# Optimization experiments

Hardware: AMD Instinct MI355X
Metric: run time of the kernel (lower is better)

The kernel has to match this reference:

```python
import jax, jax.numpy as jnp
import numpy as np

N_USERS = 20000
N_ITEMS = 30000
N = N_USERS + N_ITEMS          # total nodes
D = 64                          # embedding_dim
EXTRA = 1152                    # 768 metadata + 384 review
E = 500000                      # full-graph edges
NC = 100                        # clusters
HEADS = 2                       # per-layer GATConv heads
CG_HEADS = 4                    # GlobalGATOverClusters hard-codes heads=4
L = 2                           # num_layers
ED = 2                          # edge_dim


def _gat(x, ei, ea, lin, a_src, a_dst, lin_e, a_edge, bias, heads, nnodes):
    """PyG GATConv: add self loops (edge_attr fill='mean'), concat=False -> head mean."""
    C = a_src.shape[-1]
    loop = jnp.arange(nnodes)
    src = jnp.concatenate([ei[0], loop])
    dst = jnp.concatenate([ei[1], loop])
    ea_full = jnp.concatenate([ea, jnp.broadcast_to(ea.mean(0), (nnodes, ea.shape[1]))], 0)
    xh = (x @ lin).reshape(nnodes, heads, C)            # [N,H,C]
    asrc = (xh * a_src).sum(-1)                         # [N,H]
    adst = (xh * a_dst).sum(-1)
    eh = (ea_full @ lin_e).reshape(-1, heads, C)        # [Etot,H,C]
    ae = (eh * a_edge).sum(-1)                          # [Etot,H]
    al = jax.nn.leaky_relu(asrc[src] + adst[dst] + ae, 0.2)
    amax = jax.ops.segment_max(al, dst, num_segments=nnodes)
    ex = jnp.exp(al - amax[dst])
    s = jax.ops.segment_sum(ex, dst, num_segments=nnodes)
    w = ex / (s[dst] + 1e-16)
    out = jax.ops.segment_sum(xh[src] * w[..., None], dst, num_segments=nnodes)
    return out.mean(1) + bias


def _graph_norm(x, weight, bias, mean_scale, eps=1e-5):
    mean = x.mean(0)
    out = x - mean_scale * mean
    var = (out * out).mean(0)
    return weight * out * jax.lax.rsqrt(var + eps) + bias


def _forward(product_extra_features, user_emb, item_emb, fus_w1, fus_b1, fus_w2, fus_b2,
             full_edge_attr, gcn_w, gcn_b,
             cg_lin, cg_att_src, cg_att_dst, cg_lin_edge, cg_att_edge, cg_bias, cluster_edge_attr,
             gat_lin, gat_att_src, gat_att_dst, gat_lin_edge, gat_att_edge, gat_bias,
             gn_weight, gn_bias, gn_mean_scale,
             full_edge_index, cluster_assignment, cluster_edge_index):
    # fusion MLP on item side (dropout is identity at inference)
    h = jnp.maximum(jnp.concatenate([item_emb, product_extra_features], -1) @ fus_w1 + fus_b1, 0.0)
    enriched_items = h @ fus_w2 + fus_b2
    X = jnp.concatenate([user_emb, enriched_items], 0)  # [N, D]

    # per-cluster GCN == one GCN over intra-cluster edges + self loops;
    # nodes in clusters with zero intra edges keep original features
    ei0, ei1 = full_edge_index[0], full_edge_index[1]
    intra = cluster_assignment[ei0] == cluster_assignment[ei1]
    loop = jnp.arange(N)
    row = jnp.concatenate([ei0, loop])
    col = jnp.concatenate([ei1, loop])
    ew = jnp.concatenate([intra.astype(X.dtype), jnp.ones((N,), X.dtype)])
    deg = jax.ops.segment_sum(ew, col, num_segments=N)
    dinv = jnp.where(deg > 0, jax.lax.rsqrt(deg), 0.0)
    norm = dinv[row] * ew * dinv[col]
    xw = X @ gcn_w
    gcn_out = jax.ops.segment_sum(xw[row] * norm[:, None], col, num_segments=N) + gcn_b
    cl_has_edge = jax.ops.segment_sum(intra.astype(jnp.int32), cluster_assignment[ei0], num_segments=NC) > 0
    Xc = jnp.where(cl_has_edge[cluster_assignment][:, None], gcn_out, X)

    # mean pool per cluster
    cnt = jax.ops.segment_sum(jnp.ones((N,), X.dtype), cluster_assignment, num_segments=NC)
    pooled = jax.ops.segment_sum(Xc, cluster_assignment, num_segments=NC) / jnp.maximum(cnt, 1.0)[:, None]

    # global GAT over clusters (inter-cluster multigraph, precomputed)
    cl_upd = _gat(pooled, cluster_edge_index, cluster_edge_attr,
                  cg_lin, cg_att_src, cg_att_dst, cg_lin_edge, cg_att_edge, cg_bias, CG_HEADS, NC)
    Xcomb = Xc + cl_upd[cluster_assignment]

    # full-graph GAT stack with GraphNorm + residual ELU (dropout identity)
    for i in range(L):
        Xin = Xcomb
        g = _gat(Xcomb, full_edge_index, full_edge_attr,
                 gat_lin[i], gat_att_src[i], gat_att_dst[i],
                 gat_lin_edge[i], gat_att_edge[i], gat_bias[i], HEADS, N)
        g = _graph_norm(g, gn_weight[i], gn_bias[i], gn_mean_scale[i])
        Xcomb = jax.nn.elu(g + Xin)

    return Xcomb[:N_USERS], Xcomb[N_USERS:]


def setup_inputs() -> dict:
    rng = np.random.default_rng(0)
    fei = rng.integers(0, N, size=(2, E)).astype(np.int32)
    ca = rng.integers(0, NC, size=(N,)).astype(np.int32)
    fea = rng.random((E, ED)).astype(np.float32)
    # build_cluster_graph: one cluster edge per inter-cluster full edge
    cu, cv = ca[fei[0]], ca[fei[1]]
    m = cu != cv
    cei = np.stack([cu[m], cv[m]]).astype(np.int32)
    cea = fea[m]

    key = jax.random.key(0)
    ks = jax.random.split(key, 24)
    nrm = lambda k, shp, s=0.05: jax.random.normal(k, shp, dtype=jnp.float32) * s
    return {
        'product_extra_features': jax.random.normal(ks[0], (N_ITEMS, EXTRA), dtype=jnp.float32),
        'user_emb': nrm(ks[1], (N_USERS, D), 1.0),
        'item_emb': nrm(ks[2], (N_ITEMS, D), 1.0),
        'fus_w1': nrm(ks[3], (D + EXTRA, 2 * D)),
        'fus_b1': jnp.zeros((2 * D,), jnp.float32),
        'fus_w2': nrm(ks[4], (2 * D, D)),
        'fus_b2': jnp.zeros((D,), jnp.float32),
        'full_edge_attr': jnp.asarray(fea),
        'gcn_w': nrm(ks[5], (D, D)),
        'gcn_b': jnp.zeros((D,), jnp.float32),
        'cg_lin': nrm(ks[6], (D, CG_HEADS * D)),
        'cg_att_src': nrm(ks[7], (CG_HEADS, D)),
        'cg_att_dst': nrm(ks[8], (CG_HEADS, D)),
        'cg_lin_edge': nrm(ks[9], (ED, CG_HEADS * D)),
        'cg_att_edge': nrm(ks[10], (CG_HEADS, D)),
        'cg_bias': jnp.zeros((D,), jnp.float32),
        'cluster_edge_attr': jnp.asarray(cea),
        'gat_lin': nrm(ks[11], (L, D, HEADS * D)),
        'gat_att_src': nrm(ks[12], (L, HEADS, D)),
        'gat_att_dst': nrm(ks[13], (L, HEADS, D)),
        'gat_lin_edge': nrm(ks[14], (L, ED, HEADS * D)),
        'gat_att_edge': nrm(ks[15], (L, HEADS, D)),
        'gat_bias': jnp.zeros((L, D), jnp.float32),
        'gn_weight': jnp.ones((L, D), jnp.float32),
        'gn_bias': jnp.zeros((L, D), jnp.float32),
        'gn_mean_scale': jnp.ones((L, D), jnp.float32),
        'full_edge_index': jnp.asarray(fei),
        'cluster_assignment': jnp.asarray(ca),
        'cluster_edge_index': jnp.asarray(cei),
    }


def reference(product_extra_features, user_emb, item_emb, fus_w1, fus_b1, fus_w2, fus_b2,
              full_edge_attr, gcn_w, gcn_b,
              cg_lin, cg_att_src, cg_att_dst, cg_lin_edge, cg_att_edge, cg_bias, cluster_edge_attr,
              gat_lin, gat_att_src, gat_att_dst, gat_lin_edge, gat_att_edge, gat_bias,
              gn_weight, gn_bias, gn_mean_scale,
              full_edge_index, cluster_assignment, cluster_edge_index):
    return _forward(product_extra_features, user_emb, item_emb, fus_w1, fus_b1, fus_w2, fus_b2,
                    full_edge_attr, gcn_w, gcn_b,
                    cg_lin, cg_att_src, cg_att_dst, cg_lin_edge, cg_att_edge, cg_bias, cluster_edge_attr,
                    gat_lin, gat_att_src, gat_att_dst, gat_lin_edge, gat_att_edge, gat_bias,
                    gn_weight, gn_bias, gn_mean_scale,
                    full_edge_index, cluster_assignment, cluster_edge_index)
```

## Files before the change

### kernel.cpp

```cpp
#include <hip/hip_runtime.h>
#include <hip/hip_bf16.h>

#define N_USERS 20000
#define N_ITEMS 30000
#define NTOT    50000
#define DIM     64
#define EXTRA_D 1152
#define E_EDGES 500000
#define NC      100
#define KTOT    1216
#define KSTEPS  38
#define PPART   16

#define FEI_BLKS 128
#define CEI_BLKS 64
#define FILL_BLKS ((E_EDGES+255)/256)
#define DEG_BLKS ((NTOT+3)/4)

typedef __attribute__((ext_vector_type(8))) short short8;
typedef __attribute__((ext_vector_type(4))) float v4f;

__device__ __forceinline__ float wred_sum(float v){
#pragma unroll
  for(int o=32;o;o>>=1) v += __shfl_xor(v,o,64);
  return v;
}
__device__ __forceinline__ int wred_sumi(int v){
#pragma unroll
  for(int o=32;o;o>>=1) v += __shfl_xor(v,o,64);
  return v;
}
__device__ __forceinline__ float lrelu(float x){ return x>0.f? x : 0.2f*x; }
__device__ __forceinline__ short f2bf(float f){
  unsigned u=__float_as_uint(f);
  unsigned r=(u + 0x7FFFu + ((u>>16)&1u))>>16;
  return (short)r;
}

__global__ __launch_bounds__(256) void prep_misc_kernel(
    const float* __restrict__ u, float* __restrict__ X,
    const float* __restrict__ w1, short* __restrict__ w1t,
    const float* __restrict__ w2, short* __restrict__ w2t,
    const int* __restrict__ ca, int* __restrict__ ccnt)
{
  __shared__ int hist[NC];
  const int b=blockIdx.x, t=threadIdx.x;
  if(b < 1250){
    int i = b*256+t;
    ((float4*)X)[i] = ((const float4*)u)[i];
  } else if(b < 1858){
    int i = (b-1250)*256+t;
    int s = i>>12, rem = i&4095, n = rem>>5, kk = rem&31;
    w1t[i] = f2bf(w1[(s*32+kk)*128 + n]);
  } else if(b < 1890){
    int i = (b-1858)*256+t;
    int c = i>>7, n = i&127;
    w2t[i] = f2bf(w2[n*64+c]);
  } else {
    for(int i=t;i<NC;i+=256) hist[i]=0;
    __syncthreads();
    for(int n=(b-1890)*256+t; n<NTOT; n+=64*256) atomicAdd(&hist[ca[n]],1);
    __syncthreads();
    for(int i=t;i<NC;i+=256) if(hist[i]) atomicAdd(&ccnt[i],hist[i]);
  }
}

__global__ __launch_bounds__(256) void fusion_mfma_kernel(
    const float* __restrict__ item, const float* __restrict__ extra,
    const short* __restrict__ w1t, const float* __restrict__ b1,
    const short* __restrict__ w2t, const float* __restrict__ b2,
    float* __restrict__ X)
{
  __shared__ short As[128*40];
  __shared__ short Bs[128*40];
  __shared__ short Hs[128*136];
  const int tid = threadIdx.x;
  const int blk = blockIdx.x;
  const int w = tid>>6, lane = tid&63, quad = lane>>4, l16 = lane&15;
  const int mw = w&1, nw = w>>1;

  v4f acc[4][4];
#pragma unroll
  for(int a=0;a<4;a++)
#pragma unroll
    for(int b=0;b<4;b++) acc[a][b] = (v4f){0.f,0.f,0.f,0.f};

  const int arow = tid>>3;
  const int aoff = (tid&7)*4;
  for(int s=0;s<KSTEPS;s++){
    const int k0 = s*32;
#pragma unroll
    for(int it=0;it<4;it++){
      int r = arow + it*32;
      int col = k0 + aoff;
      int gr = blk*128 + r; if(gr >= N_ITEMS) gr = N_ITEMS-1;
      float4 v = (col < DIM) ? *(const float4*)(item + (size_t)gr*DIM + col)
                             : *(const float4*)(extra + (size_t)gr*EXTRA_D + (col-DIM));
      short4 bv; bv.x=f2bf(v.x); bv.y=f2bf(v.y); bv.z=f2bf(v.z); bv.w=f2bf(v.w);
      *(short4*)&As[r*40 + aoff] = bv;
    }
#pragma unroll
    for(int it=0;it<2;it++){
      int idx = tid + it*256;
      int4 v = *(const int4*)(w1t + (size_t)s*4096 + idx*8);
      int n = idx>>2, kk = (idx&3)*8;
      *(int4*)&Bs[n*40 + kk] = v;
    }
    __syncthreads();
    short8 af[4], bf_[4];
#pragma unroll
    for(int i=0;i<4;i++){
      int m = mw*64 + i*16 + l16;
      af[i]  = *(const short8*)&As[m*40 + quad*8];
      int n = nw*64 + i*16 + l16;
      bf_[i] = *(const short8*)&Bs[n*40 + quad*8];
    }
#pragma unroll
    for(int mi=0;mi<4;mi++)
#pragma unroll
      for(int ni=0;ni<4;ni++)
        acc[mi][ni] = __builtin_amdgcn_mfma_f32_16x16x32_bf16(af[mi], bf_[ni], acc[mi][ni], 0,0,0);
    __syncthreads();
  }

#pragma unroll
  for(int ni=0;ni<4;ni++){
    int n = nw*64 + ni*16 + l16;
    float bias = b1[n];
#pragma unroll
    for(int mi=0;mi<4;mi++){
      int mbase = mw*64 + mi*16 + quad*4;
#pragma unroll
      for(int r=0;r<4;r++){
        float hv = fmaxf(acc[mi][ni][r] + bias, 0.f);
        Hs[(mbase+r)*136 + n] = f2bf(hv);
      }
    }
  }
  __syncthreads();

  v4f acc2[2][4];
#pragma unroll
  for(int a=0;a<2;a++)
#pragma unroll
    for(int b=0;b<4;b++) acc2[a][b] = (v4f){0.f,0.f,0.f,0.f};
#pragma unroll
  for(int ks=0;ks<4;ks++){
    short8 ha[2];
#pragma unroll
    for(int mi=0;mi<2;mi++){
      int m = w*32 + mi*16 + l16;
      ha[mi] = *(const short8*)&Hs[m*136 + ks*32 + quad*8];
    }
#pragma unroll
    for(int ni=0;ni<4;ni++){
      int c = ni*16 + l16;
      short8 wb = *(const short8*)(w2t + c*128 + ks*32 + quad*8);
#pragma unroll
      for(int mi=0;mi<2;mi++)
        acc2[mi][ni] = __builtin_amdgcn_mfma_f32_16x16x32_bf16(ha[mi], wb, acc2[mi][ni], 0,0,0);
    }
  }
#pragma unroll
  for(int ni=0;ni<4;ni++){
    int c = ni*16 + l16;
    float b2v = b2[c];
#pragma unroll
    for(int mi=0;mi<2;mi++){
      int mbase = w*32 + mi*16 + quad*4;
#pragma unroll
      for(int r=0;r<4;r++){
        int row = blk*128 + mbase + r;
        if(row < N_ITEMS) X[(size_t)(N_USERS+row)*64 + c] = acc2[mi][ni][r] + b2v;
      }
    }
  }
}

__global__ __launch_bounds__(256) void edge_pass_kernel(
    const int* __restrict__ fei, const float* __restrict__ fea, const int* __restrict__ ca,
    int* __restrict__ cnt_dst, int* __restrict__ clflag, float2* __restrict__ partA,
    const int* __restrict__ cei, const float* __restrict__ cea, int Ec,
    int* __restrict__ ccnt_dst, float2* __restrict__ partB)
{
  __shared__ int hist[NC];
  __shared__ float2 w4[4];
  const int b=blockIdx.x, t=threadIdx.x;
  const int lane=t&63, wv=t>>6;
  if(b < FEI_BLKS){
    float a0=0.f,a1=0.f;
    for(int e=b*256+t; e<E_EDGES; e+=FEI_BLKS*256){
      int s=fei[e], d=fei[E_EDGES+e];
      atomicAdd(&cnt_dst[d],1);
      int cs=ca[s];
      if(cs==ca[d]) clflag[cs]=1;
      float2 v=*(const float2*)(fea+2*e);
      a0+=v.x; a1+=v.y;
    }
    a0=wred_sum(a0); a1=wred_sum(a1);
    if(lane==0) w4[wv]=make_float2(a0,a1);
    __syncthreads();
    if(t==0){ float2 r=w4[0]; for(int i=1;i<4;i++){r.x+=w4[i].x; r.y+=w4[i].y;} partA[b]=r; }
  } else {
    int bb=b-FEI_BLKS;
    for(int i=t;i<NC;i+=256) hist[i]=0;
    __syncthreads();
    float a0=0.f,a1=0.f;
    for(int e=bb*256+t; e<Ec; e+=CEI_BLKS*256){
      atomicAdd(&hist[cei[Ec+e]],1);
      float2 v=*(const float2*)(cea+2*e);
      a0+=v.x; a1+=v.y;
    }
    a0=wred_sum(a0); a1=wred_sum(a1);
    if(lane==0) w4[wv]=make_float2(a0,a1);
    __syncthreads();
    if(t==0){ float2 r=w4[0]; for(int i=1;i<4;i++){r.x+=w4[i].x; r.y+=w4[i].y;} partB[bb]=r; }
    for(int i=t;i<NC;i+=256) if(hist[i]) atomicAdd(&ccnt_dst[i],hist[i]);
  }
}

__global__ void prep_small_kernel(const float2* __restrict__ partA, const float2* __restrict__ partB,
    int Ec,
    const float* __restrict__ cg_le, const float* __restrict__ cg_ae,
    const float* __restrict__ gat_le, const float* __restrict__ gat_ae,
    float* __restrict__ coefs)
{
  int tid=threadIdx.x; int lane=tid&63; int wv=tid>>6;
  {
    int hh=wv;
    float v0 = cg_le[hh*64+lane]*cg_ae[hh*64+lane];
    float v1 = cg_le[256 + hh*64+lane]*cg_ae[hh*64+lane];
    v0=wred_sum(v0); v1=wred_sum(v1);
    if(lane==0){ coefs[8+hh]=v0; coefs[12+hh]=v1; }
  }
  {
    int l=wv>>1, hh=wv&1;
    float v0 = gat_le[l*256 + hh*64+lane]     * gat_ae[l*128+hh*64+lane];
    float v1 = gat_le[l*256 + 128 + hh*64+lane]* gat_ae[l*128+hh*64+lane];
    v0=wred_sum(v0); v1=wred_sum(v1);
    if(lane==0){ coefs[16+l*2+hh]=v0; coefs[20+l*2+hh]=v1; }
  }
  __syncthreads();
  if(wv==0){
    float2 v=partA[lane], v2=partA[64+lane];
    float sx=wred_sum(v.x+v2.x), sy=wred_sum(v.y+v2.y);
    if(lane==0){ coefs[4]=sx/(float)E_EDGES; coefs[5]=sy/(float)E_EDGES; }
  }
  if(wv==1){
    float2 v=partB[lane];
    float sx=wred_sum(v.x), sy=wred_sum(v.y);
    if(lane==0){ coefs[6]=sx/(float)Ec; coefs[7]=sy/(float)Ec; }
  }
}

__global__ __launch_bounds__(1024) void scan1_kernel(const int* __restrict__ cnt,
    int* __restrict__ incl, int* __restrict__ bsum){
  __shared__ int s[1024];
  int i = blockIdx.x*1024 + threadIdx.x;
  int v = (i<NTOT)? cnt[i]+1 : 0;
  s[threadIdx.x]=v; __syncthreads();
  for(int off=1; off<1024; off<<=1){
    int t = (threadIdx.x>=off)? s[threadIdx.x-off] : 0;
    __syncthreads();
    s[threadIdx.x]+=t;
    __syncthreads();
  }
  if(i<NTOT) incl[i]=s[threadIdx.x];
  if(threadIdx.x==1023) bsum[blockIdx.x]=s[1023];
}
__global__ void small_scans_kernel(int* __restrict__ bsum, int nb,
    const int* __restrict__ ccnt_dst, int* __restrict__ coffs, int* __restrict__ cfillp){
  int lane=threadIdx.x;
  if(blockIdx.x==0){
    int v = (lane<nb)? bsum[lane]:0;
#pragma unroll
    for(int o=1;o<64;o<<=1){ int t=__shfl_up(v,o,64); if(lane>=o) v+=t; }
    if(lane<nb) bsum[lane]=v;
  } else {
    int v0 = (2*lane<NC)? ccnt_dst[2*lane]:0;
    int v1 = (2*lane+1<NC)? ccnt_dst[2*lane+1]:0;
    int pair=v0+v1;
    int sc=pair;
#pragma unroll
    for(int o=1;o<64;o<<=1){ int t2=__shfl_up(sc,o,64); if(lane>=o) sc+=t2; }
    int excl = sc - pair;
    if(2*lane<NC){ coffs[2*lane]=excl; cfillp[2*lane]=excl; }
    if(2*lane+1<NC){ coffs[2*lane+1]=excl+v0; cfillp[2*lane+1]=excl+v0; }
    if(lane==63) coffs[NC]=sc;
  }
}
__global__ void scan3_kernel(const int* __restrict__ incl, const int* __restrict__ cnt,
    const int* __restrict__ bsum, int* __restrict__ offs, int* __restrict__ fillptr,
    const float* __restrict__ coefs, int4* __restrict__ slot){
  int i=blockIdx.x*256+threadIdx.x;
  if(i<NTOT){
    int blk=i>>10;
    int prev = blk? bsum[blk-1]:0;
    int c=cnt[i];
    int start = prev + incl[i] - (c+1);
    offs[i]=start; fillptr[i]=start;
    slot[start+c]=make_int4(i,__float_as_int(coefs[4]),__float_as_int(coefs[5]),0);
  }
  if(i==0) offs[NTOT]=E_EDGES+NTOT;
}
__global__ __launch_bounds__(256) void fill_both_kernel(
    const int* __restrict__ fei, const float* __restrict__ fea,
    int* __restrict__ fillptr, int4* __restrict__ slot,
    const int* __restrict__ cei, const float* __restrict__ cea, int Ec,
    int* __restrict__ cfillp, int* __restrict__ cslot_src, float2* __restrict__ cslot_ea)
{
  __shared__ int hist[NC];
  __shared__ int base[NC];
  const int b=blockIdx.x, t=threadIdx.x;
  if(b<FILL_BLKS){
    int e=b*256+t;
    if(e<E_EDGES){
      int dst=fei[E_EDGES+e], src=fei[e];
      int pos=atomicAdd(&fillptr[dst],1);
      float2 v=*(const float2*)(fea+2*e);
      slot[pos]=make_int4(src,__float_as_int(v.x),__float_as_int(v.y),0);
    }
  } else {
    int bb=b-FILL_BLKS;
    const int chunk=(Ec+127)/128;
    const int beg=bb*chunk;
    const int end=min(beg+chunk,Ec);
    for(int i=t;i<NC;i+=256) hist[i]=0;
    __syncthreads();
    for(int e=beg+t;e<end;e+=256) atomicAdd(&hist[cei[Ec+e]],1);
    __syncthreads();
    for(int i=t;i<NC;i+=256){
      int h=hist[i];
      base[i] = h ? atomicAdd(&cfillp[i],h) : 0;
      hist[i]=0;
    }
    __syncthreads();
    for(int e=beg+t;e<end;e+=256){
      int d=cei[Ec+e];
      int pos = base[d] + atomicAdd(&hist[d],1);
      cslot_src[pos]=cei[e];
      cslot_ea[pos]=make_float2(cea[2*e],cea[2*e+1]);
    }
  }
}

__global__ __launch_bounds__(256) void gcn_pre_kernel(const int* __restrict__ offs,
    const int4* __restrict__ slot, const int* __restrict__ ca, float* __restrict__ dinv,
    const float* __restrict__ X, const float* __restrict__ gw, float* __restrict__ xw){
  __shared__ float Wl[64*64];
  __shared__ float rowb[4][64];
  const int b=blockIdx.x;
  const int lane=threadIdx.x&63, wv=threadIdx.x>>6;
  if(b<DEG_BLKS){
    int n = b*4+wv; if(n>=NTOT) return;
    int beg=offs[n], end=offs[n+1], myca=ca[n];
    int c=0;
    for(int j=beg+lane;j<end;j+=64) c += (ca[slot[j].x]==myca)?1:0;
    c = wred_sumi(c);
    if(lane==0) dinv[n]=rsqrtf((float)c);
  } else {
    int bb=b-DEG_BLKS;
    for(int i=threadIdx.x;i<4096;i+=256) Wl[i]=gw[i];
    __syncthreads();
    for(int r=bb*4+wv; r<NTOT; r+=1024*4){
      rowb[wv][lane]=X[(size_t)r*64+lane];
      float acc=0.f;
#pragma unroll 8
      for(int k=0;k<64;k++) acc+=rowb[wv][k]*Wl[k*64+lane];
      xw[(size_t)r*64+lane]=acc;
    }
  }
}
__global__ __launch_bounds__(256) void gcn_agg_kernel(const float* __restrict__ X,
    const float* __restrict__ xw, const float* __restrict__ gcn_b,
    const int* __restrict__ offs, const int4* __restrict__ slot, const int* __restrict__ ca,
    const float* __restrict__ dinv, const int* __restrict__ flag,
    float* __restrict__ Xc, float* __restrict__ psum){
  __shared__ float2 stg[4][64];
  int lane=threadIdx.x&63, wv=threadIdx.x>>6;
  int n=blockIdx.x*4+wv; if(n>=NTOT) return;
  int beg=offs[n], end=offs[n+1], myca=ca[n];
  float acc=0.f;
  for(int c0=beg;c0<end;c0+=64){
    int j=c0+lane;
    float coef=0.f; int s=0;
    if(j<end){
      s=slot[j].x;
      if(ca[s]==myca) coef=dinv[s];
    }
    stg[wv][lane]=make_float2(__int_as_float(s),coef);
    unsigned long long bal=__ballot(coef!=0.f);
    while(bal){
      int k=__builtin_ctzll(bal); bal&=bal-1;
      float2 sc=stg[wv][k];
      acc += sc.y * xw[(size_t)__float_as_int(sc.x)*64+lane];
    }
  }
  float gout = dinv[n]*acc + gcn_b[lane];
  float xc = flag[myca] ? gout : X[(size_t)n*64+lane];
  Xc[(size_t)n*64+lane]=xc;
  atomicAdd(&psum[(size_t)(blockIdx.x&(PPART-1))*NC*64 + myca*64+lane], xc);
}

__global__ __launch_bounds__(256) void cluster_prep_kernel(const float* __restrict__ psum,
    const int* __restrict__ ccnt, const float* __restrict__ cg_lin,
    const float* __restrict__ as_, const float* __restrict__ ad_,
    float* __restrict__ xh_c, float* __restrict__ asrc_c, float* __restrict__ adst_c){
  __shared__ float prow[64];
  const int c=blockIdx.x, t=threadIdx.x;
  if(t<64){
    float a=0.f;
#pragma unroll
    for(int p=0;p<PPART;p++) a += psum[(size_t)p*NC*64 + c*64 + t];
    prow[t]=a/fmaxf((float)ccnt[c],1.f);
  }
  __syncthreads();
  float acc=0.f;
#pragma unroll 8
  for(int k=0;k<64;k++) acc += prow[k]*cg_lin[k*256+t];
  xh_c[c*256+t]=acc;
  int lane=t&63, hh=t>>6;
  float s=wred_sum(acc*as_[hh*64+lane]);
  float d=wred_sum(acc*ad_[hh*64+lane]);
  if(lane==0){ asrc_c[c*4+hh]=s; adst_c[c*4+hh]=d; }
}
__global__ __launch_bounds__(256) void cluster_agg_kernel(
    const int* __restrict__ coffs, const int* __restrict__ cslot_src, const float2* __restrict__ cslot_ea,
    const float* __restrict__ asrc_c, const float* __restrict__ adst_c, const float* __restrict__ coefs,
    const float* __restrict__ xh_c, const float* __restrict__ cg_bias, float* __restrict__ cl_upd)
{
  __shared__ float sas[NC*4];
  __shared__ float sW[NC*4];
  __shared__ float ssum[4];
  __shared__ float red[4][64];
  const int c=blockIdx.x, t=threadIdx.x;
  for(int i=t;i<NC*4;i+=256){ sas[i]=asrc_c[i]; sW[i]=0.f; }
  __syncthreads();
  float ad[4], A0[4], A1[4];
#pragma unroll
  for(int h=0;h<4;h++){ ad[h]=adst_c[c*4+h]; A0[h]=coefs[8+h]; A1[h]=coefs[12+h]; }
  const int beg=coffs[c], end=coffs[c+1];
  for(int j=beg+t;j<end;j+=256){
    int s=cslot_src[j]; float2 e=cslot_ea[j];
#pragma unroll
    for(int h=0;h<4;h++){
      float al=lrelu(sas[s*4+h]+ad[h]+e.x*A0[h]+e.y*A1[h]);
      atomicAdd(&sW[s*4+h], expf(al));
    }
  }
  if(t<4){
    float al=lrelu(sas[c*4+t]+ad[t]+coefs[6]*A0[t]+coefs[7]*A1[t]);
    atomicAdd(&sW[c*4+t], expf(al));
  }
  __syncthreads();
  const int h=t>>6, lane=t&63;
  float p=0.f;
  if(lane<NC)    p += sW[lane*4+h];
  if(lane+64<NC) p += sW[(lane+64)*4+h];
  p=wred_sum(p);
  if(lane==0) ssum[h]=p+1e-16f;
  __syncthreads();
  float inv=1.f/ssum[h];
  float acc=0.f;
  for(int s=0;s<NC;s++) acc += sW[s*4+h]*xh_c[s*256+h*64+lane];
  red[h][lane]=acc*inv;
  __syncthreads();
  if(t<64) cl_upd[c*64+t]=0.25f*(red[0][t]+red[1][t]+red[2][t]+red[3][t])+cg_bias[t];
}

__global__ __launch_bounds__(256) void gat_xh0_kernel(const float* __restrict__ Xc,
    const float* __restrict__ cl_upd, const int* __restrict__ ca,
    const float* __restrict__ lin, const float* __restrict__ att_s, const float* __restrict__ att_d,
    float2* __restrict__ xh2, float* __restrict__ asrc, float* __restrict__ adst,
    float* __restrict__ Xa){
  __shared__ __align__(16) float Wl[64*128];
  __shared__ float rowb[4][64];
  int t=threadIdx.x;
  for(int i=t;i<8192;i+=256) Wl[i]=lin[i];
  __syncthreads();
  int lane=t&63, wv=t>>6;
  float as0=att_s[lane], as1=att_s[64+lane], ad0=att_d[lane], ad1=att_d[64+lane];
  for(int r=blockIdx.x*4+wv; r<NTOT; r+=gridDim.x*4){
    float xv = Xc[(size_t)r*64+lane] + cl_upd[ca[r]*64+lane];
    Xa[(size_t)r*64+lane]=xv;
    rowb[wv][lane]=xv;
    float x0=0.f,x1=0.f;
#pragma unroll 8
    for(int k=0;k<64;k++){ float q=rowb[wv][k]; x0+=q*Wl[k*128+lane]; x1+=q*Wl[k*128+64+lane]; }
    xh2[(size_t)r*64+lane]=make_float2(x0,x1);
    float p0=wred_sum(x0*as0);
    float p1=wred_sum(x1*as1);
    float q0=wred_sum(x0*ad0);
    float q1=wred_sum(x1*ad1);
    if(lane==0){ asrc[2*r]=p0; asrc[2*r+1]=p1; adst[2*r]=q0; adst[2*r+1]=q1; }
  }
}
__global__ __launch_bounds__(256) void gat_xh1_kernel(const float* __restrict__ g,
    const float* __restrict__ Xres, const float* __restrict__ stats,
    const float* __restrict__ gnw, const float* __restrict__ gnb, const float* __restrict__ gnms,
    const float* __restrict__ lin, const float* __restrict__ att_s, const float* __restrict__ att_d,
    float2* __restrict__ xh2, float* __restrict__ asrc, float* __restrict__ adst,
    float* __restrict__ Xb){
  __shared__ __align__(16) float Wl[64*128];
  __shared__ float rowb[4][64];
  int t=threadIdx.x;
  for(int i=t;i<8192;i+=256) Wl[i]=lin[i];
  __syncthreads();
  int lane=t&63, wv=t>>6;
  const float invN = 1.f/(float)NTOT;
  float m=stats[lane]*invN;
  float mm=gnms[lane]*m;
  float gwv=rsqrtf(stats[64+lane]*invN - 2.f*mm*m + mm*mm + 1e-5f)*gnw[lane];
  float gbv=gnb[lane];
  float as0=att_s[lane], as1=att_s[64+lane], ad0=att_d[lane], ad1=att_d[64+lane];
  for(int r=blockIdx.x*4+wv; r<NTOT; r+=gridDim.x*4){
    float z=(g[(size_t)r*64+lane]-mm)*gwv+gbv + Xres[(size_t)r*64+lane];
    float xv = z>0.f? z : expf(z)-1.f;
    Xb[(size_t)r*64+lane]=xv;
    rowb[wv][lane]=xv;
    float x0=0.f,x1=0.f;
#pragma unroll 8
    for(int k=0;k<64;k++){ float q=rowb[wv][k]; x0+=q*Wl[k*128+lane]; x1+=q*Wl[k*128+64+lane]; }
    xh2[(size_t)r*64+lane]=make_float2(x0,x1);
    float p0=wred_sum(x0*as0);
    float p1=wred_sum(x1*as1);
    float q0=wred_sum(x0*ad0);
    float q1=wred_sum(x1*ad1);
    if(lane==0){ asrc[2*r]=p0; asrc[2*r+1]=p1; adst[2*r]=q0; adst[2*r+1]=q1; }
  }
}

__global__ __launch_bounds__(256) void gat_agg_kernel(const float2* __restrict__ xh2,
    const float2* __restrict__ asrc, const float2* __restrict__ adst,
    const int* __restrict__ offs, const int4* __restrict__ slot,
    const float* __restrict__ coefs, int layer, const float* __restrict__ bias,
    float* __restrict__ g){
  __shared__ float4 stg[4][64];
  int lane=threadIdx.x&63, wv=threadIdx.x>>6;
  int n=blockIdx.x*4+wv; if(n>=NTOT) return;
  float A00=coefs[16+layer*2+0], A01=coefs[16+layer*2+1];
  float A10=coefs[20+layer*2+0], A11=coefs[20+layer*2+1];
  int beg=offs[n], end=offs[n+1];
  float2 adn=adst[n];
  float s0=0.f,s1=0.f,acc0=0.f,acc1=0.f;
  for(int c0=beg;c0<end;c0+=64){
    int j=c0+lane;
    float ex0=0.f,ex1=0.f; int s=0;
    if(j<end){
      int4 sl=slot[j];
      s=sl.x;
      float e0=__int_as_float(sl.y), e1=__int_as_float(sl.z);
      float2 a=asrc[s];
      ex0=expf(lrelu(a.x+adn.x+e0*A00+e1*A10));
      ex1=expf(lrelu(a.y+adn.y+e0*A01+e1*A11));
    }
    s0+=ex0; s1+=ex1;
    stg[wv][lane]=make_float4(__int_as_float(s),ex0,ex1,0.f);
    int cnt=min(64,end-c0);
    int k=0;
    for(; k+4<=cnt; k+=4){
      float4 w0=stg[wv][k], w1=stg[wv][k+1], w2=stg[wv][k+2], w3=stg[wv][k+3];
      float2 x0=xh2[(size_t)__float_as_int(w0.x)*64+lane];
      float2 x1=xh2[(size_t)__float_as_int(w1.x)*64+lane];
      float2 x2=xh2[(size_t)__float_as_int(w2.x)*64+lane];
      float2 x3=xh2[(size_t)__float_as_int(w3.x)*64+lane];
      acc0 += w0.y*x0.x + w1.y*x1.x + w2.y*x2.x + w3.y*x3.x;
      acc1 += w0.z*x0.y + w1.z*x1.y + w2.z*x2.y + w3.z*x3.y;
    }
    for(; k<cnt; k++){
      float4 ws=stg[wv][k];
      float2 xv=xh2[(size_t)__float_as_int(ws.x)*64+lane];
      acc0 += ws.y*xv.x;
      acc1 += ws.z*xv.y;
    }
  }
  s0=wred_sum(s0); s1=wred_sum(s1);
  g[(size_t)n*64+lane]=0.5f*(acc0/(s0+1e-16f)+acc1/(s1+1e-16f))+bias[lane];
}
__global__ __launch_bounds__(256) void stats_kernel(const float* __restrict__ g,
    float* __restrict__ stats){
  __shared__ float s1[64], s2[64];
  int t=threadIdx.x;
  if(t<64){s1[t]=0.f;s2[t]=0.f;}
  __syncthreads();
  float a0=0.f,a1=0.f,a2=0.f,a3=0.f,b0=0.f,b1=0.f,b2=0.f,b3=0.f;
  int i0=blockIdx.x*256+t;
  for(int i=i0;i<NTOT*16;i+=gridDim.x*256){
    float4 v=((const float4*)g)[i];
    a0+=v.x;a1+=v.y;a2+=v.z;a3+=v.w;
    b0+=v.x*v.x;b1+=v.y*v.y;b2+=v.z*v.z;b3+=v.w*v.w;
  }
  int d0=(i0&15)*4;
  atomicAdd(&s1[d0],a0); atomicAdd(&s1[d0+1],a1); atomicAdd(&s1[d0+2],a2); atomicAdd(&s1[d0+3],a3);
  atomicAdd(&s2[d0],b0); atomicAdd(&s2[d0+1],b1); atomicAdd(&s2[d0+2],b2); atomicAdd(&s2[d0+3],b3);
  __syncthreads();
  if(t<64) atomicAdd(&stats[t],s1[t]);
  else if(t<128) atomicAdd(&stats[t],s2[t-64]);
}
__global__ __launch_bounds__(256) void gnorm_elu_kernel(const float* __restrict__ g,
    const float* __restrict__ Xin, const float* __restrict__ stats,
    const float* __restrict__ gw, const float* __restrict__ gb, const float* __restrict__ gms,
    float* __restrict__ outp){
  const float invN = 1.f/(float)NTOT;
  int i0=blockIdx.x*256+threadIdx.x;
  int d0=(i0&15)*4;
  float mmv[4],gwv[4],gbv[4];
#pragma unroll
  for(int j=0;j<4;j++){
    int d=d0+j;
    float m=stats[d]*invN;
    float mm=gms[d]*m;
    mmv[j]=mm;
    gwv[j]=rsqrtf(stats[64+d]*invN-2.f*mm*m+mm*mm+1e-5f)*gw[d];
    gbv[j]=gb[d];
  }
  for(int i=i0;i<NTOT*16;i+=gridDim.x*256){
    float4 gv=((const float4*)g)[i];
    float4 xv=((const float4*)Xin)[i];
    float4 o; float z;
    z=(gv.x-mmv[0])*gwv[0]+gbv[0]+xv.x; o.x = z>0.f? z : expf(z)-1.f;
    z=(gv.y-mmv[1])*gwv[1]+gbv[1]+xv.y; o.y = z>0.f? z : expf(z)-1.f;
    z=(gv.z-mmv[2])*gwv[2]+gbv[2]+xv.z; o.z = z>0.f? z : expf(z)-1.f;
    z=(gv.w-mmv[3])*gwv[3]+gbv[3]+xv.w; o.w = z>0.f? z : expf(z)-1.f;
    ((float4*)outp)[i]=o;
  }
}

extern "C" void kernel_launch(void* const* d_in, const int* in_sizes, int n_in,
                              void* d_out, int out_size, void* d_ws, size_t ws_size,
                              hipStream_t stream)
{
  const float* extra = (const float*)d_in[0];
  const float* user  = (const float*)d_in[1];
  const float* item  = (const float*)d_in[2];
  const float* fw1 = (const float*)d_in[3];
  const float* fb1 = (const float*)d_in[4];
  const float* fw2 = (const float*)d_in[5];
  const float* fb2 = (const float*)d_in[6];
  const float* fea = (const float*)d_in[7];
  const float* gcn_w = (const float*)d_in[8];
  const float* gcn_b = (const float*)d_in[9];
  const float* cg_lin = (const float*)d_in[10];
  const float* cg_as = (const float*)d_in[11];
  const float* cg_ad = (const float*)d_in[12];
  const float* cg_le = (const float*)d_in[13];
  const float* cg_ae = (const float*)d_in[14];
  const float* cg_bias = (const float*)d_in[15];
  const float* cea = (const float*)d_in[16];
  const float* gat_lin = (const float*)d_in[17];
  const float* gat_as = (const float*)d_in[18];
  const float* gat_ad = (const float*)d_in[19];
  const float* gat_le = (const float*)d_in[20];
  const float* gat_ae = (const float*)d_in[21];
  const float* gat_bias = (const float*)d_in[22];
  const float* gn_w = (const float*)d_in[23];
  const float* gn_b = (const float*)d_in[24];
  const float* gn_ms = (const float*)d_in[25];
  const int* fei = (const int*)d_in[26];
  const int* ca  = (const int*)d_in[27];
  const int* cei = (const int*)d_in[28];
  const int Ec = in_sizes[16]/2;
  float* outp = (float*)d_out;

  char* w = (char*)d_ws;
  auto alloc=[&](size_t b)->char*{ char* p=w; w += (b+255)&~(size_t)255; return p; };

  char* z0 = w;
  int* cnt_dst = (int*)alloc((size_t)NTOT*4);
  int* clflag = (int*)alloc(NC*4);
  int* ccnt = (int*)alloc(NC*4);
  int* ccnt_dst = (int*)alloc(NC*4);
  float* psum = (float*)alloc((size_t)PPART*NC*64*4);
  float* stats0 = (float*)alloc(128*4);
  float* stats1 = (float*)alloc(128*4);
  size_t zbytes = (size_t)(w - z0);

  float2* partA = (float2*)alloc(128*8);
  float2* partB = (float2*)alloc(64*8);
  float* coefs = (float*)alloc(32*4);
  int* offs = (int*)alloc((size_t)(NTOT+1)*4);
  int* incl = (int*)alloc((size_t)NTOT*4);
  int* bsum = (int*)alloc(64*4);
  int* fillptr = (int*)alloc((size_t)NTOT*4);
  int4* slot = (int4*)alloc((size_t)(E_EDGES+NTOT)*16);
  int* coffs = (int*)alloc((size_t)(NC+1)*4);
  int* cfillp = (int*)alloc((size_t)NC*4);
  int* cslot_src = (int*)alloc((size_t)E_EDGES*4);
  float2* cslot_ea = (float2*)alloc((size_t)E_EDGES*8);
  float* dinv = (float*)alloc((size_t)NTOT*4);
  float* xh_c = (float*)alloc(NC*256*4);
  float* asrc_c = (float*)alloc(NC*4*4);
  float* adst_c = (float*)alloc(NC*4*4);
  float* cl_upd = (float*)alloc(NC*64*4);
  float* asrc = (float*)alloc((size_t)NTOT*2*4);
  float* adst = (float*)alloc((size_t)NTOT*2*4);
  short* w1t = (short*)alloc((size_t)KSTEPS*4096*2);
  short* w2t = (short*)alloc((size_t)64*128*2);
  float* bufA = (float*)alloc((size_t)NTOT*64*4);
  float* bufB = (float*)alloc((size_t)NTOT*64*4);
  float* bufC = (float*)alloc((size_t)NTOT*64*4);
  float* bufD = (float*)alloc((size_t)NTOT*64*4);
  float* bufE = (float*)alloc((size_t)NTOT*128*4);

  float* X  = bufA; float* g  = bufA;
  float* Xc = bufB;
  float* xw = bufC; float* Xb = bufC;
  float* Xa = bufD;
  float2* xh2 = (float2*)bufE;

  hipMemsetAsync(z0, 0, zbytes, stream);

  prep_misc_kernel<<<1954,256,0,stream>>>(user, X, fw1, w1t, fw2, w2t, ca, ccnt);
  fusion_mfma_kernel<<<(N_ITEMS+127)/128,256,0,stream>>>(item, extra, w1t, fb1, w2t, fb2, X);

  edge_pass_kernel<<<FEI_BLKS+CEI_BLKS,256,0,stream>>>(fei, fea, ca, cnt_dst, clflag, partA,
                                                       cei, cea, Ec, ccnt_dst, partB);
  prep_small_kernel<<<1,256,0,stream>>>(partA, partB, Ec, cg_le, cg_ae, gat_le, gat_ae, coefs);

  scan1_kernel<<<(NTOT+1023)/1024,1024,0,stream>>>(cnt_dst, incl, bsum);
  small_scans_kernel<<<2,64,0,stream>>>(bsum, (NTOT+1023)/1024, ccnt_dst, coffs, cfillp);
  scan3_kernel<<<(NTOT+255)/256,256,0,stream>>>(incl, cnt_dst, bsum, offs, fillptr, coefs, slot);
  fill_both_kernel<<<FILL_BLKS+128,256,0,stream>>>(fei, fea, fillptr, slot,
                                                   cei, cea, Ec, cfillp, cslot_src, cslot_ea);

  gcn_pre_kernel<<<DEG_BLKS+1024,256,0,stream>>>(offs, slot, ca, dinv, X, gcn_w, xw);
  gcn_agg_kernel<<<DEG_BLKS,256,0,stream>>>(X, xw, gcn_b, offs, slot, ca, dinv, clflag, Xc, psum);
  cluster_prep_kernel<<<NC,256,0,stream>>>(psum, ccnt, cg_lin, cg_as, cg_ad, xh_c, asrc_c, adst_c);
  cluster_agg_kernel<<<NC,256,0,stream>>>(coffs, cslot_src, cslot_ea, asrc_c, adst_c, coefs,
                                          xh_c, cg_bias, cl_upd);

  gat_xh0_kernel<<<1024,256,0,stream>>>(Xc, cl_upd, ca, gat_lin, gat_as, gat_ad,
                                        xh2, asrc, adst, Xa);
  gat_agg_kernel<<<DEG_BLKS,256,0,stream>>>(xh2, (const float2*)asrc, (const float2*)adst,
                                            offs, slot, coefs, 0, gat_bias, g);
  stats_kernel<<<128,256,0,stream>>>(g, stats0);
  gat_xh1_kernel<<<1024,256,0,stream>>>(g, Xa, stats0, gn_w, gn_b, gn_ms,
                                        gat_lin+64*128, gat_as+128, gat_ad+128,
                                        xh2, asrc, adst, Xb);
  gat_agg_kernel<<<DEG_BLKS,256,0,stream>>>(xh2, (const float2*)asrc, (const float2*)adst,
                                            offs, slot, coefs, 1, gat_bias+64, g);
  stats_kernel<<<128,256,0,stream>>>(g, stats1);
  gnorm_elu_kernel<<<512,256,0,stream>>>(g, Xb, stats1, gn_w+64, gn_b+64, gn_ms+64, outp);
}
```

Before: 712.4 us.

## Merge preprocessing kernels, shrink edge slots to int2, compute GCN degree via atomics

Result: no change. 703.2 us (-1.3%).

```diff
diff --git a/kernel.cpp b/kernel.cpp
--- a/kernel.cpp
+++ b/kernel.cpp
@@ -12,8 +12,17 @@
 #define KSTEPS  38
 #define PPART   16
 
-#define FEI_BLKS 128
-#define CEI_BLKS 64
+#define B_COPY 1250
+#define B_W1   608
+#define B_W2   32
+#define B_CC   64
+#define B_FEI  128
+#define B_CEI  64
+#define PREP_GRID (B_COPY+B_W1+B_W2+B_CC+B_FEI+B_CEI)
+
+#define FUS_BLKS ((N_ITEMS+127)/128)
+#define SCAN1_BLKS ((NTOT+1023)/1024)
+#define SC3_BLKS ((NTOT+255)/256)
 #define FILL_BLKS ((E_EDGES+255)/256)
 #define DEG_BLKS ((NTOT+3)/4)
 
@@ -36,150 +45,18 @@
   unsigned r=(u + 0x7FFFu + ((u>>16)&1u))>>16;
   return (short)r;
 }
-
-__global__ __launch_bounds__(256) void prep_misc_kernel(
+__device__ __forceinline__ unsigned pack_bf2(float x, float y){
+  return (unsigned)(unsigned short)f2bf(x) | ((unsigned)(unsigned short)f2bf(y)<<16);
+}
+
+__global__ __launch_bounds__(256) void prep_all_kernel(
     const float* __restrict__ u, float* __restrict__ X,
     const float* __restrict__ w1, short* __restrict__ w1t,
     const float* __restrict__ w2, short* __restrict__ w2t,
-    const int* __restrict__ ca, int* __restrict__ ccnt)
-{
-  __shared__ int hist[NC];
-  const int b=blockIdx.x, t=threadIdx.x;
-  if(b < 1250){
-    int i = b*256+t;
-    ((float4*)X)[i] = ((const float4*)u)[i];
-  } else if(b < 1858){
-    int i = (b-1250)*256+t;
-    int s = i>>12, rem = i&4095, n = rem>>5, kk = rem&31;
-    w1t[i] = f2bf(w1[(s*32+kk)*128 + n]);
-  } else if(b < 1890){
-    int i = (b-1858)*256+t;
-    int c = i>>7, n = i&127;
-    w2t[i] = f2bf(w2[n*64+c]);
-  } else {
-    for(int i=t;i<NC;i+=256) hist[i]=0;
-    __syncthreads();
-    for(int n=(b-1890)*256+t; n<NTOT; n+=64*256) atomicAdd(&hist[ca[n]],1);
-    __syncthreads();
-    for(int i=t;i<NC;i+=256) if(hist[i]) atomicAdd(&ccnt[i],hist[i]);
-  }
-}
-
-__global__ __launch_bounds__(256) void fusion_mfma_kernel(
-    const float* __restrict__ item, const float* __restrict__ extra,
-    const short* __restrict__ w1t, const float* __restrict__ b1,
-    const short* __restrict__ w2t, const float* __restrict__ b2,
-    float* __restrict__ X)
-{
-  __shared__ short As[128*40];
-  __shared__ short Bs[128*40];
-  __shared__ short Hs[128*136];
-  const int tid = threadIdx.x;
-  const int blk = blockIdx.x;
-  const int w = tid>>6, lane = tid&63, quad = lane>>4, l16 = lane&15;
-  const int mw = w&1, nw = w>>1;
-
-  v4f acc[4][4];
-#pragma unroll
-  for(int a=0;a<4;a++)
-#pragma unroll
-    for(int b=0;b<4;b++) acc[a][b] = (v4f){0.f,0.f,0.f,0.f};
-
-  const int arow = tid>>3;
-  const int aoff = (tid&7)*4;
-  for(int s=0;s<KSTEPS;s++){
-    const int k0 = s*32;
-#pragma unroll
-    for(int it=0;it<4;it++){
-      int r = arow + it*32;
-      int col = k0 + aoff;
-      int gr = blk*128 + r; if(gr >= N_ITEMS) gr = N_ITEMS-1;
-      float4 v = (col < DIM) ? *(const float4*)(item + (size_t)gr*DIM + col)
-                             : *(const float4*)(extra + (size_t)gr*EXTRA_D + (col-DIM));
-      short4 bv; bv.x=f2bf(v.x); bv.y=f2bf(v.y); bv.z=f2bf(v.z); bv.w=f2bf(v.w);
-      *(short4*)&As[r*40 + aoff] = bv;
-    }
-#pragma unroll
-    for(int it=0;it<2;it++){
-      int idx = tid + it*256;
-      int4 v = *(const int4*)(w1t + (size_t)s*4096 + idx*8);
-      int n = idx>>2, kk = (idx&3)*8;
-      *(int4*)&Bs[n*40 + kk] = v;
-    }
-    __syncthreads();
-    short8 af[4], bf_[4];
-#pragma unroll
-    for(int i=0;i<4;i++){
-      int m = mw*64 + i*16 + l16;
-      af[i]  = *(const short8*)&As[m*40 + quad*8];
-      int n = nw*64 + i*16 + l16;
-      bf_[i] = *(const short8*)&Bs[n*40 + quad*8];
-    }
-#pragma unroll
-    for(int mi=0;mi<4;mi++)
-#pragma unroll
-      for(int ni=0;ni<4;ni++)
-        acc[mi][ni] = __builtin_amdgcn_mfma_f32_16x16x32_bf16(af[mi], bf_[ni], acc[mi][ni], 0,0,0);
-    __syncthreads();
-  }
-
-#pragma unroll
-  for(int ni=0;ni<4;ni++){
-    int n = nw*64 + ni*16 + l16;
-    float bias = b1[n];
-#pragma unroll
-    for(int mi=0;mi<4;mi++){
-      int mbase = mw*64 + mi*16 + quad*4;
-#pragma unroll
-      for(int r=0;r<4;r++){
-        float hv = fmaxf(acc[mi][ni][r] + bias, 0.f);
-        Hs[(mbase+r)*136 + n] = f2bf(hv);
-      }
-    }
-  }
-  __syncthreads();
-
-  v4f acc2[2][4];
-#pragma unroll
-  for(int a=0;a<2;a++)
-#pragma unroll
-    for(int b=0;b<4;b++) acc2[a][b] = (v4f){0.f,0.f,0.f,0.f};
-#pragma unroll
-  for(int ks=0;ks<4;ks++){
-    short8 ha[2];
-#pragma unroll
-    for(int mi=0;mi<2;mi++){
-      int m = w*32 + mi*16 + l16;
-      ha[mi] = *(const short8*)&Hs[m*136 + ks*32 + quad*8];
-    }
-#pragma unroll
-    for(int ni=0;ni<4;ni++){
-      int c = ni*16 + l16;
-      short8 wb = *(const short8*)(w2t + c*128 + ks*32 + quad*8);
-#pragma unroll
-      for(int mi=0;mi<2;mi++)
-        acc2[mi][ni] = __builtin_amdgcn_mfma_f32_16x16x32_bf16(ha[mi], wb, acc2[mi][ni], 0,0,0);
-    }
-  }
-#pragma unroll
-  for(int ni=0;ni<4;ni++){
-    int c = ni*16 + l16;
-    float b2v = b2[c];
-#pragma unroll
-    for(int mi=0;mi<2;mi++){
-      int mbase = w*32 + mi*16 + quad*4;
-#pragma unroll
-      for(int r=0;r<4;r++){
-        int row = blk*128 + mbase + r;
-        if(row < N_ITEMS) X[(size_t)(N_USERS+row)*64 + c] = acc2[mi][ni][r] + b2v;
-      }
-    }
-  }
-}
-
-__global__ __launch_bounds__(256) void edge_pass_kernel(
-    const int* __restrict__ fei, const float* __restrict__ fea, const int* __restrict__ ca,
-    int* __restrict__ cnt_dst, int* __restrict__ clflag, float2* __restrict__ partA,
+    const int* __restrict__ ca, int* __restrict__ ccnt,
+    const int* __restrict__ fei, const float* __restrict__ fea,
+    int* __restrict__ cnt_dst, int* __restrict__ clflag, int* __restrict__ degI,
+    float2* __restrict__ partA,
     const int* __restrict__ cei, const float* __restrict__ cea, int Ec,
     int* __restrict__ ccnt_dst, float2* __restrict__ partB)
 {
@@ -187,26 +64,45 @@
   __shared__ float2 w4[4];
   const int b=blockIdx.x, t=threadIdx.x;
   const int lane=t&63, wv=t>>6;
-  if(b < FEI_BLKS){
+  if(b < B_COPY){
+    int i = b*256+t;
+    ((float4*)X)[i] = ((const float4*)u)[i];
+  } else if(b < B_COPY+B_W1){
+    int i = (b-B_COPY)*256+t;
+    int s = i>>12, rem = i&4095, n = rem>>5, kk = rem&31;
+    w1t[i] = f2bf(w1[(s*32+kk)*128 + n]);
+  } else if(b < B_COPY+B_W1+B_W2){
+    int i = (b-B_COPY-B_W1)*256+t;
+    int c = i>>7, n = i&127;
+    w2t[i] = f2bf(w2[n*64+c]);
+  } else if(b < B_COPY+B_W1+B_W2+B_CC){
+    int bb = b-(B_COPY+B_W1+B_W2);
+    for(int i=t;i<NC;i+=256) hist[i]=0;
+    __syncthreads();
+    for(int n=bb*256+t; n<NTOT; n+=B_CC*256) atomicAdd(&hist[ca[n]],1);
+    __syncthreads();
+    for(int i=t;i<NC;i+=256) if(hist[i]) atomicAdd(&ccnt[i],hist[i]);
+  } else if(b < B_COPY+B_W1+B_W2+B_CC+B_FEI){
+    int bb = b-(B_COPY+B_W1+B_W2+B_CC);
     float a0=0.f,a1=0.f;
-    for(int e=b*256+t; e<E_EDGES; e+=FEI_BLKS*256){
+    for(int e=bb*256+t; e<E_EDGES; e+=B_FEI*256){
       int s=fei[e], d=fei[E_EDGES+e];
       atomicAdd(&cnt_dst[d],1);
       int cs=ca[s];
-      if(cs==ca[d]) clflag[cs]=1;
+      if(cs==ca[d]){ clflag[cs]=1; atomicAdd(&degI[d],1); }
       float2 v=*(const float2*)(fea+2*e);
       a0+=v.x; a1+=v.y;
     }
     a0=wred_sum(a0); a1=wred_sum(a1);
     if(lane==0) w4[wv]=make_float2(a0,a1);
     __syncthreads();
-    if(t==0){ float2 r=w4[0]; for(int i=1;i<4;i++){r.x+=w4[i].x; r.y+=w4[i].y;} partA[b]=r; }
+    if(t==0){ float2 r=w4[0]; for(int i=1;i<4;i++){r.x+=w4[i].x; r.y+=w4[i].y;} partA[bb]=r; }
   } else {
-    int bb=b-FEI_BLKS;
+    int bb = b-(B_COPY+B_W1+B_W2+B_CC+B_FEI);
     for(int i=t;i<NC;i+=256) hist[i]=0;
     __syncthreads();
     float a0=0.f,a1=0.f;
-    for(int e=bb*256+t; e<Ec; e+=CEI_BLKS*256){
+    for(int e=bb*256+t; e<Ec; e+=B_CEI*256){
       atomicAdd(&hist[cei[Ec+e]],1);
       float2 v=*(const float2*)(cea+2*e);
       a0+=v.x; a1+=v.y;
@@ -219,93 +115,235 @@
   }
 }
 
-__global__ void prep_small_kernel(const float2* __restrict__ partA, const float2* __restrict__ partB,
-    int Ec,
+__global__ __launch_bounds__(256) void fus_scan_kernel(
+    const float* __restrict__ item, const float* __restrict__ extra,
+    const short* __restrict__ w1t, const float* __restrict__ b1,
+    const short* __restrict__ w2t, const float* __restrict__ b2,
+    float* __restrict__ X,
+    const float2* __restrict__ partA, const float2* __restrict__ partB, int Ec,
     const float* __restrict__ cg_le, const float* __restrict__ cg_ae,
     const float* __restrict__ gat_le, const float* __restrict__ gat_ae,
-    float* __restrict__ coefs)
+    float* __restrict__ coefs,
+    const int* __restrict__ cnt_dst, int* __restrict__ incl, int* __restrict__ bsum)
 {
-  int tid=threadIdx.x; int lane=tid&63; int wv=tid>>6;
-  {
-    int hh=wv;
-    float v0 = cg_le[hh*64+lane]*cg_ae[hh*64+lane];
-    float v1 = cg_le[256 + hh*64+lane]*cg_ae[hh*64+lane];
-    v0=wred_sum(v0); v1=wred_sum(v1);
-    if(lane==0){ coefs[8+hh]=v0; coefs[12+hh]=v1; }
-  }
-  {
-    int l=wv>>1, hh=wv&1;
-    float v0 = gat_le[l*256 + hh*64+lane]     * gat_ae[l*128+hh*64+lane];
-    float v1 = gat_le[l*256 + 128 + hh*64+lane]* gat_ae[l*128+hh*64+lane];
-    v0=wred_sum(v0); v1=wred_sum(v1);
-    if(lane==0){ coefs[16+l*2+hh]=v0; coefs[20+l*2+hh]=v1; }
-  }
-  __syncthreads();
-  if(wv==0){
-    float2 v=partA[lane], v2=partA[64+lane];
-    float sx=wred_sum(v.x+v2.x), sy=wred_sum(v.y+v2.y);
-    if(lane==0){ coefs[4]=sx/(float)E_EDGES; coefs[5]=sy/(float)E_EDGES; }
-  }
-  if(wv==1){
-    float2 v=partB[lane];
-    float sx=wred_sum(v.x), sy=wred_sum(v.y);
-    if(lane==0){ coefs[6]=sx/(float)Ec; coefs[7]=sy/(float)Ec; }
-  }
-}
-
-__global__ __launch_bounds__(1024) void scan1_kernel(const int* __restrict__ cnt,
-    int* __restrict__ incl, int* __restrict__ bsum){
-  __shared__ int s[1024];
-  int i = blockIdx.x*1024 + threadIdx.x;
-  int v = (i<NTOT)? cnt[i]+1 : 0;
-  s[threadIdx.x]=v; __syncthreads();
-  for(int off=1; off<1024; off<<=1){
-    int t = (threadIdx.x>=off)? s[threadIdx.x-off] : 0;
-    __syncthreads();
-    s[threadIdx.x]+=t;
-    __syncthreads();
-  }
-  if(i<NTOT) incl[i]=s[threadIdx.x];
-  if(threadIdx.x==1023) bsum[blockIdx.x]=s[1023];
-}
-__global__ void small_scans_kernel(int* __restrict__ bsum, int nb,
-    const int* __restrict__ ccnt_dst, int* __restrict__ coffs, int* __restrict__ cfillp){
-  int lane=threadIdx.x;
-  if(blockIdx.x==0){
-    int v = (lane<nb)? bsum[lane]:0;
-#pragma unroll
-    for(int o=1;o<64;o<<=1){ int t=__shfl_up(v,o,64); if(lane>=o) v+=t; }
-    if(lane<nb) bsum[lane]=v;
+  __shared__ short As[128*40];
+  __shared__ short Bs[128*40];
+  __shared__ short Hs[128*136];
+  __shared__ int ssc[256];
+  const int tid = threadIdx.x;
+  const int b = blockIdx.x;
+  if(b < FUS_BLKS){
+    const int blk = b;
+    const int w = tid>>6, lane = tid&63, quad = lane>>4, l16 = lane&15;
+    const int mw = w&1, nw = w>>1;
+
+    v4f acc[4][4];
+#pragma unroll
+    for(int a=0;a<4;a++)
+#pragma unroll
+      for(int c=0;c<4;c++) acc[a][c] = (v4f){0.f,0.f,0.f,0.f};
+
+    const int arow = tid>>3;
+    const int aoff = (tid&7)*4;
+    for(int s=0;s<KSTEPS;s++){
+      const int k0 = s*32;
+#pragma unroll
+      for(int it=0;it<4;it++){
+        int r = arow + it*32;
+        int col = k0 + aoff;
+        int gr = blk*128 + r; if(gr >= N_ITEMS) gr = N_ITEMS-1;
+        float4 v = (col < DIM) ? *(const float4*)(item + (size_t)gr*DIM + col)
+                               : *(const float4*)(extra + (size_t)gr*EXTRA_D + (col-DIM));
+        short4 bv; bv.x=f2bf(v.x); bv.y=f2bf(v.y); bv.z=f2bf(v.z); bv.w=f2bf(v.w);
+        *(short4*)&As[r*40 + aoff] = bv;
+      }
+#pragma unroll
+      for(int it=0;it<2;it++){
+        int idx = tid + it*256;
+        int4 v = *(const int4*)(w1t + (size_t)s*4096 + idx*8);
+        int n = idx>>2, kk = (idx&3)*8;
+        *(int4*)&Bs[n*40 + kk] = v;
+      }
+      __syncthreads();
+      short8 af[4], bf_[4];
+#pragma unroll
+      for(int i=0;i<4;i++){
+        int m = mw*64 + i*16 + l16;
+        af[i]  = *(const short8*)&As[m*40 + quad*8];
+        int n = nw*64 + i*16 + l16;
+        bf_[i] = *(const short8*)&Bs[n*40 + quad*8];
+      }
+#pragma unroll
+      for(int mi=0;mi<4;mi++)
+#pragma unroll
+        for(int ni=0;ni<4;ni++)
+          acc[mi][ni] = __builtin_amdgcn_mfma_f32_16x16x32_bf16(af[mi], bf_[ni], acc[mi][ni], 0,0,0);
+      __syncthreads();
+    }
+
+#pragma unroll
+    for(int ni=0;ni<4;ni++){
+      int n = nw*64 + ni*16 + l16;
+      float bias = b1[n];
+#pragma unroll
+      for(int mi=0;mi<4;mi++){
+        int mbase = mw*64 + mi*16 + quad*4;
+#pragma unroll
+        for(int r=0;r<4;r++){
+          float hv = fmaxf(acc[mi][ni][r] + bias, 0.f);
+          Hs[(mbase+r)*136 + n] = f2bf(hv);
+        }
+      }
+    }
+    __syncthreads();
+
+    v4f acc2[2][4];
+#pragma unroll
+    for(int a=0;a<2;a++)
+#pragma unroll
+      for(int c=0;c<4;c++) acc2[a][c] = (v4f){0.f,0.f,0.f,0.f};
+#pragma unroll
+    for(int ks=0;ks<4;ks++){
+      short8 ha[2];
+#pragma unroll
+      for(int mi=0;mi<2;mi++){
+        int m = w*32 + mi*16 + l16;
+        ha[mi] = *(const short8*)&Hs[m*136 + ks*32 + quad*8];
+      }
+#pragma unroll
+      for(int ni=0;ni<4;ni++){
+        int c = ni*16 + l16;
+        short8 wb = *(const short8*)(w2t + c*128 + ks*32 + quad*8);
+#pragma unroll
+        for(int mi=0;mi<2;mi++)
+          acc2[mi][ni] = __builtin_amdgcn_mfma_f32_16x16x32_bf16(ha[mi], wb, acc2[mi][ni], 0,0,0);
+      }
+    }
+#pragma unroll
+    for(int ni=0;ni<4;ni++){
+      int c = ni*16 + l16;
+      float b2v = b2[c];
+#pragma unroll
+      for(int mi=0;mi<2;mi++){
+        int mbase = w*32 + mi*16 + quad*4;
+#pragma unroll
+        for(int r=0;r<4;r++){
+          int row = blk*128 + mbase + r;
+          if(row < N_ITEMS) X[(size_t)(N_USERS+row)*64 + c] = acc2[mi][ni][r] + b2v;
+        }
+      }
+    }
+  } else if(b == FUS_BLKS){
+    int lane=tid&63; int wv=tid>>6;
+    {
+      int hh=wv;
+      float v0 = cg_le[hh*64+lane]*cg_ae[hh*64+lane];
+      float v1 = cg_le[256 + hh*64+lane]*cg_ae[hh*64+lane];
+      v0=wred_sum(v0); v1=wred_sum(v1);
+      if(lane==0){ coefs[8+hh]=v0; coefs[12+hh]=v1; }
+    }
+    {
+      int l=wv>>1, hh=wv&1;
+      float v0 = gat_le[l*256 + hh*64+lane]     * gat_ae[l*128+hh*64+lane];
+      float v1 = gat_le[l*256 + 128 + hh*64+lane]* gat_ae[l*128+hh*64+lane];
+      v0=wred_sum(v0); v1=wred_sum(v1);
+      if(lane==0){ coefs[16+l*2+hh]=v0; coefs[20+l*2+hh]=v1; }
+    }
+    __syncthreads();
+    if(wv==0){
+      float2 v=partA[lane], v2=partA[64+lane];
+      float sx=wred_sum(v.x+v2.x), sy=wred_sum(v.y+v2.y);
+      if(lane==0){ coefs[4]=sx/(float)E_EDGES; coefs[5]=sy/(float)E_EDGES; }
+    }
+    if(wv==1){
+      float2 v=partB[lane];
+      float sx=wred_sum(v.x), sy=wred_sum(v.y);
+      if(lane==0){ coefs[6]=sx/(float)Ec; coefs[7]=sy/(float)Ec; }
+    }
   } else {
-    int v0 = (2*lane<NC)? ccnt_dst[2*lane]:0;
-    int v1 = (2*lane+1<NC)? ccnt_dst[2*lane+1]:0;
-    int pair=v0+v1;
-    int sc=pair;
-#pragma unroll
-    for(int o=1;o<64;o<<=1){ int t2=__shfl_up(sc,o,64); if(lane>=o) sc+=t2; }
-    int excl = sc - pair;
-    if(2*lane<NC){ coffs[2*lane]=excl; cfillp[2*lane]=excl; }
-    if(2*lane+1<NC){ coffs[2*lane+1]=excl+v0; cfillp[2*lane+1]=excl+v0; }
-    if(lane==63) coffs[NC]=sc;
-  }
-}
-__global__ void scan3_kernel(const int* __restrict__ incl, const int* __restrict__ cnt,
+    int sb = b-FUS_BLKS-1;
+    int base = sb*1024 + tid*4;
+    int a0=(base  <NTOT)?cnt_dst[base  ]+1:0;
+    int a1=(base+1<NTOT)?cnt_dst[base+1]+1:0;
+    int a2=(base+2<NTOT)?cnt_dst[base+2]+1:0;
+    int a3=(base+3<NTOT)?cnt_dst[base+3]+1:0;
+    int l1=a0+a1, l2=l1+a2, l3=l2+a3;
+    ssc[tid]=l3; __syncthreads();
+    for(int off=1;off<256;off<<=1){
+      int v=(tid>=off)?ssc[tid-off]:0; __syncthreads();
+      ssc[tid]+=v; __syncthreads();
+    }
+    int prev = tid? ssc[tid-1]:0;
+    if(base  <NTOT) incl[base  ]=prev+a0;
+    if(base+1<NTOT) incl[base+1]=prev+l1;
+    if(base+2<NTOT) incl[base+2]=prev+l2;
+    if(base+3<NTOT) incl[base+3]=prev+l3;
+    if(tid==255) bsum[sb]=ssc[255];
+  }
+}
+
+__global__ __launch_bounds__(256) void mid_kernel(
+    const int* __restrict__ incl, const int* __restrict__ cnt,
     const int* __restrict__ bsum, int* __restrict__ offs, int* __restrict__ fillptr,
-    const float* __restrict__ coefs, int4* __restrict__ slot){
-  int i=blockIdx.x*256+threadIdx.x;
-  if(i<NTOT){
-    int blk=i>>10;
-    int prev = blk? bsum[blk-1]:0;
-    int c=cnt[i];
-    int start = prev + incl[i] - (c+1);
-    offs[i]=start; fillptr[i]=start;
-    slot[start+c]=make_int4(i,__float_as_int(coefs[4]),__float_as_int(coefs[5]),0);
-  }
-  if(i==0) offs[NTOT]=E_EDGES+NTOT;
-}
-__global__ __launch_bounds__(256) void fill_both_kernel(
+    const float* __restrict__ coefs, int2* __restrict__ slot2,
+    const int* __restrict__ degI, float* __restrict__ dinv,
+    const int* __restrict__ ccnt_dst, int* __restrict__ coffs, int* __restrict__ cfillp,
+    const float* __restrict__ X, const float* __restrict__ gw, float* __restrict__ xw)
+{
+  __shared__ float Wl[64*64];
+  __shared__ float rowb[4][64];
+  __shared__ int sprev;
+  const int b=blockIdx.x, t=threadIdx.x;
+  if(b < SC3_BLKS){
+    int blk10 = b>>2;
+    if(t<64){
+      int v = (t<blk10)? bsum[t] : 0;
+      v = wred_sumi(v);
+      if(t==0) sprev=v;
+    }
+    __syncthreads();
+    unsigned pk = pack_bf2(coefs[4], coefs[5]);
+    int i = b*256+t;
+    if(i<NTOT){
+      int c=cnt[i];
+      int start = sprev + incl[i] - (c+1);
+      offs[i]=start; fillptr[i]=start;
+      slot2[start+c]=make_int2(i,(int)pk);
+      dinv[i]=rsqrtf((float)(degI[i]+1));
+    }
+    if(i==0) offs[NTOT]=E_EDGES+NTOT;
+  } else if(b == SC3_BLKS){
+    if(t<64){
+      int lane=t;
+      int v0 = (2*lane<NC)? ccnt_dst[2*lane]:0;
+      int v1 = (2*lane+1<NC)? ccnt_dst[2*lane+1]:0;
+      int pair=v0+v1;
+      int sc=pair;
+#pragma unroll
+      for(int o=1;o<64;o<<=1){ int t2=__shfl_up(sc,o,64); if(lane>=o) sc+=t2; }
+      int excl = sc - pair;
+      if(2*lane<NC){ coffs[2*lane]=excl; cfillp[2*lane]=excl; }
+      if(2*lane+1<NC){ coffs[2*lane+1]=excl+v0; cfillp[2*lane+1]=excl+v0; }
+      if(lane==63) coffs[NC]=sc;
+    }
+  } else {
+    int bb=b-SC3_BLKS-1;
+    const int lane=t&63, wv=t>>6;
+    for(int i=t;i<4096;i+=256) Wl[i]=gw[i];
+    __syncthreads();
+    for(int r=bb*4+wv; r<NTOT; r+=1024*4){
+      rowb[wv][lane]=X[(size_t)r*64+lane];
+      float acc=0.f;
+#pragma unroll 8
+      for(int k=0;k<64;k++) acc+=rowb[wv][k]*Wl[k*64+lane];
+      xw[(size_t)r*64+lane]=acc;
+    }
+  }
+}
+
+__global__ __launch_bounds__(256) void fill_kernel(
     const int* __restrict__ fei, const float* __restrict__ fea,
-    int* __restrict__ fillptr, int4* __restrict__ slot,
+    int* __restrict__ fillptr, int2* __restrict__ slot2,
     const int* __restrict__ cei, const float* __restrict__ cea, int Ec,
     int* __restrict__ cfillp, int* __restrict__ cslot_src, float2* __restrict__ cslot_ea)
 {
@@ -318,7 +356,7 @@
       int dst=fei[E_EDGES+e], src=fei[e];
       int pos=atomicAdd(&fillptr[dst],1);
       float2 v=*(const float2*)(fea+2*e);
-      slot[pos]=make_int4(src,__float_as_int(v.x),__float_as_int(v.y),0);
+      slot2[pos]=make_int2(src,(int)pack_bf2(v.x,v.y));
     }
   } else {
     int bb=b-FILL_BLKS;
@@ -344,36 +382,9 @@
   }
 }
 
-__global__ __launch_bounds__(256) void gcn_pre_kernel(const int* __restrict__ offs,
-    const int4* __restrict__ slot, const int* __restrict__ ca, float* __restrict__ dinv,
-    const float* __restrict__ X, const float* __restrict__ gw, float* __restrict__ xw){
-  __shared__ float Wl[64*64];
-  __shared__ float rowb[4][64];
-  const int b=blockIdx.x;
-  const int lane=threadIdx.x&63, wv=threadIdx.x>>6;
-  if(b<DEG_BLKS){
-    int n = b*4+wv; if(n>=NTOT) return;
-    int beg=offs[n], end=offs[n+1], myca=ca[n];
-    int c=0;
-    for(int j=beg+lane;j<end;j+=64) c += (ca[slot[j].x]==myca)?1:0;
-    c = wred_sumi(c);
-    if(lane==0) dinv[n]=rsqrtf((float)c);
-  } else {
-    int bb=b-DEG_BLKS;
-    for(int i=threadIdx.x;i<4096;i+=256) Wl[i]=gw[i];
-    __syncthreads();
-    for(int r=bb*4+wv; r<NTOT; r+=1024*4){
-      rowb[wv][lane]=X[(size_t)r*64+lane];
-      float acc=0.f;
-#pragma unroll 8
-      for(int k=0;k<64;k++) acc+=rowb[wv][k]*Wl[k*64+lane];
-      xw[(size_t)r*64+lane]=acc;
-    }
-  }
-}
 __global__ __launch_bounds__(256) void gcn_agg_kernel(const float* __restrict__ X,
     const float* __restrict__ xw, const float* __restrict__ gcn_b,
-    const int* __restrict__ offs, const int4* __restrict__ slot, const int* __restrict__ ca,
+    const int* __restrict__ offs, const int2* __restrict__ slot2, const int* __restrict__ ca,
     const float* __restrict__ dinv, const int* __restrict__ flag,
     float* __restrict__ Xc, float* __restrict__ psum){
   __shared__ float2 stg[4][64];
@@ -385,7 +396,7 @@
     int j=c0+lane;
     float coef=0.f; int s=0;
     if(j<end){
-      s=slot[j].x;
+      s=slot2[j].x;
       if(ca[s]==myca) coef=dinv[s];
     }
     stg[wv][lane]=make_float2(__int_as_float(s),coef);
@@ -445,12 +456,12 @@
 #pragma unroll
     for(int h=0;h<4;h++){
       float al=lrelu(sas[s*4+h]+ad[h]+e.x*A0[h]+e.y*A1[h]);
-      atomicAdd(&sW[s*4+h], expf(al));
+      atomicAdd(&sW[s*4+h], __expf(al));
     }
   }
   if(t<4){
     float al=lrelu(sas[c*4+t]+ad[t]+coefs[6]*A0[t]+coefs[7]*A1[t]);
-    atomicAdd(&sW[c*4+t], expf(al));
+    atomicAdd(&sW[c*4+t], __expf(al));
   }
   __syncthreads();
   const int h=t>>6, lane=t&63;
@@ -515,7 +526,7 @@
   float as0=att_s[lane], as1=att_s[64+lane], ad0=att_d[lane], ad1=att_d[64+lane];
   for(int r=blockIdx.x*4+wv; r<NTOT; r+=gridDim.x*4){
     float z=(g[(size_t)r*64+lane]-mm)*gwv+gbv + Xres[(size_t)r*64+lane];
-    float xv = z>0.f? z : expf(z)-1.f;
+    float xv = z>0.f? z : __expf(z)-1.f;
     Xb[(size_t)r*64+lane]=xv;
     rowb[wv][lane]=xv;
     float x0=0.f,x1=0.f;
@@ -532,7 +543,7 @@
 
 __global__ __launch_bounds__(256) void gat_agg_kernel(const float2* __restrict__ xh2,
     const float2* __restrict__ asrc, const float2* __restrict__ adst,
-    const int* __restrict__ offs, const int4* __restrict__ slot,
+    const int* __restrict__ offs, const int2* __restrict__ slot2,
     const float* __restrict__ coefs, int layer, const float* __restrict__ bias,
     float* __restrict__ g){
   __shared__ float4 stg[4][64];
@@ -547,12 +558,14 @@
     int j=c0+lane;
     float ex0=0.f,ex1=0.f; int s=0;
     if(j<end){
-      int4 sl=slot[j];
+      int2 sl=slot2[j];
       s=sl.x;
-      float e0=__int_as_float(sl.y), e1=__int_as_float(sl.z);
+      unsigned p=(unsigned)sl.y;
+      float e0=__uint_as_float(p<<16);
+      float e1=__uint_as_float(p&0xffff0000u);
       float2 a=asrc[s];
-      ex0=expf(lrelu(a.x+adn.x+e0*A00+e1*A10));
-      ex1=expf(lrelu(a.y+adn.y+e0*A01+e1*A11));
+      ex0=__expf(lrelu(a.x+adn.x+e0*A00+e1*A10));
+      ex1=__expf(lrelu(a.y+adn.y+e0*A01+e1*A11));
     }
     s0+=ex0; s1+=ex1;
     stg[wv][lane]=make_float4(__int_as_float(s),ex0,ex1,0.f);
@@ -618,10 +631,10 @@
     float4 gv=((const float4*)g)[i];
     float4 xv=((const float4*)Xin)[i];
     float4 o; float z;
-    z=(gv.x-mmv[0])*gwv[0]+gbv[0]+xv.x; o.x = z>0.f? z : expf(z)-1.f;
-    z=(gv.y-mmv[1])*gwv[1]+gbv[1]+xv.y; o.y = z>0.f? z : expf(z)-1.f;
-    z=(gv.z-mmv[2])*gwv[2]+gbv[2]+xv.z; o.z = z>0.f? z : expf(z)-1.f;
-    z=(gv.w-mmv[3])*gwv[3]+gbv[3]+xv.w; o.w = z>0.f? z : expf(z)-1.f;
+    z=(gv.x-mmv[0])*gwv[0]+gbv[0]+xv.x; o.x = z>0.f? z : __expf(z)-1.f;
+    z=(gv.y-mmv[1])*gwv[1]+gbv[1]+xv.y; o.y = z>0.f? z : __expf(z)-1.f;
+    z=(gv.z-mmv[2])*gwv[2]+gbv[2]+xv.z; o.z = z>0.f? z : __expf(z)-1.f;
+    z=(gv.w-mmv[3])*gwv[3]+gbv[3]+xv.w; o.w = z>0.f? z : __expf(z)-1.f;
     ((float4*)outp)[i]=o;
   }
 }
@@ -667,6 +680,7 @@
 
   char* z0 = w;
   int* cnt_dst = (int*)alloc((size_t)NTOT*4);
+  int* degI = (int*)alloc((size_t)NTOT*4);
   int* clflag = (int*)alloc(NC*4);
   int* ccnt = (int*)alloc(NC*4);
   int* ccnt_dst = (int*)alloc(NC*4);
@@ -682,7 +696,7 @@
   int* incl = (int*)alloc((size_t)NTOT*4);
   int* bsum = (int*)alloc(64*4);
   int* fillptr = (int*)alloc((size_t)NTOT*4);
-  int4* slot = (int4*)alloc((size_t)(E_EDGES+NTOT)*16);
+  int2* slot2 = (int2*)alloc((size_t)(E_EDGES+NTOT)*8);
   int* coffs = (int*)alloc((size_t)(NC+1)*4);
   int* cfillp = (int*)alloc((size_t)NC*4);
   int* cslot_src = (int*)alloc((size_t)E_EDGES*4);
@@ -710,21 +724,19 @@
 
   hipMemsetAsync(z0, 0, zbytes, stream);
 
-  prep_misc_kernel<<<1954,256,0,stream>>>(user, X, fw1, w1t, fw2, w2t, ca, ccnt);
-  fusion_mfma_kernel<<<(N_ITEMS+127)/128,256,0,stream>>>(item, extra, w1t, fb1, w2t, fb2, X);
-
-  edge_pass_kernel<<<FEI_BLKS+CEI_BLKS,256,0,stream>>>(fei, fea, ca, cnt_dst, clflag, partA,
-                                                       cei, cea, Ec, ccnt_dst, partB);
-  prep_small_kernel<<<1,256,0,stream>>>(partA, partB, Ec, cg_le, cg_ae, gat_le, gat_ae, coefs);
-
-  scan1_kernel<<<(NTOT+1023)/1024,1024,0,stream>>>(cnt_dst, incl, bsum);
-  small_scans_kernel<<<2,64,0,stream>>>(bsum, (NTOT+1023)/1024, ccnt_dst, coffs, cfillp);
-  scan3_kernel<<<(NTOT+255)/256,256,0,stream>>>(incl, cnt_dst, bsum, offs, fillptr, coefs, slot);
-  fill_both_kernel<<<FILL_BLKS+128,256,0,stream>>>(fei, fea, fillptr, slot,
-                                                   cei, cea, Ec, cfillp, cslot_src, cslot_ea);
-
-  gcn_pre_kernel<<<DEG_BLKS+1024,256,0,stream>>>(offs, slot, ca, dinv, X, gcn_w, xw);
-  gcn_agg_kernel<<<DEG_BLKS,256,0,stream>>>(X, xw, gcn_b, offs, slot, ca, dinv, clflag, Xc, psum);
+  prep_all_kernel<<<PREP_GRID,256,0,stream>>>(user, X, fw1, w1t, fw2, w2t, ca, ccnt,
+                                              fei, fea, cnt_dst, clflag, degI, partA,
+                                              cei, cea, Ec, ccnt_dst, partB);
+  fus_scan_kernel<<<FUS_BLKS+1+SCAN1_BLKS,256,0,stream>>>(item, extra, w1t, fb1, w2t, fb2, X,
+                                              partA, partB, Ec, cg_le, cg_ae, gat_le, gat_ae, coefs,
+                                              cnt_dst, incl, bsum);
+  mid_kernel<<<SC3_BLKS+1+1024,256,0,stream>>>(incl, cnt_dst, bsum, offs, fillptr, coefs, slot2,
+                                              degI, dinv, ccnt_dst, coffs, cfillp,
+                                              X, gcn_w, xw);
+  fill_kernel<<<FILL_BLKS+128,256,0,stream>>>(fei, fea, fillptr, slot2,
+                                              cei, cea, Ec, cfillp, cslot_src, cslot_ea);
+
+  gcn_agg_kernel<<<DEG_BLKS,256,0,stream>>>(X, xw, gcn_b, offs, slot2, ca, dinv, clflag, Xc, psum);
   cluster_prep_kernel<<<NC,256,0,stream>>>(psum, ccnt, cg_lin, cg_as, cg_ad, xh_c, asrc_c, adst_c);
   cluster_agg_kernel<<<NC,256,0,stream>>>(coffs, cslot_src, cslot_ea, asrc_c, adst_c, coefs,
                                           xh_c, cg_bias, cl_upd);
@@ -732,13 +744,13 @@
   gat_xh0_kernel<<<1024,256,0,stream>>>(Xc, cl_upd, ca, gat_lin, gat_as, gat_ad,
                                         xh2, asrc, adst, Xa);
   gat_agg_kernel<<<DEG_BLKS,256,0,stream>>>(xh2, (const float2*)asrc, (const float2*)adst,
-                                            offs, slot, coefs, 0, gat_bias, g);
+                                            offs, slot2, coefs, 0, gat_bias, g);
   stats_kernel<<<128,256,0,stream>>>(g, stats0);
   gat_xh1_kernel<<<1024,256,0,stream>>>(g, Xa, stats0, gn_w, gn_b, gn_ms,
                                         gat_lin+64*128, gat_as+128, gat_ad+128,
                                         xh2, asrc, adst, Xb);
   gat_agg_kernel<<<DEG_BLKS,256,0,stream>>>(xh2, (const float2*)asrc, (const float2*)adst,
-                                            offs, slot, coefs, 1, gat_bias+64, g);
+                                            offs, slot2, coefs, 1, gat_bias+64, g);
   stats_kernel<<<128,256,0,stream>>>(g, stats1);
   gnorm_elu_kernel<<<512,256,0,stream>>>(g, Xb, stats1, gn_w+64, gn_b+64, gn_ms+64, outp);
 }
```
